# Kernel optimization log

Hardware: AMD Instinct MI355X
Metric: run time of the kernel (lower is better)

## Reference

```python
import jax, jax.numpy as jnp
import numpy as np
from jax import lax

EPS = 1e-6
NUM_BANDS = 128


def setup_inputs() -> dict:
    key = jax.random.key(0)
    kx, = jax.random.split(key, 1)
    B, C, F, T = 32, 1, NUM_BANDS, 6000
    x = jax.random.uniform(kx, (B, C, F, T), dtype=jnp.float32)  # nonneg spectrogram energies
    # parameters per band, initialized as in PCEN.__init__ (s=0.025, alpha=delta=r=1.0)
    log_s = jnp.full((F,), np.log(0.025), dtype=jnp.float32)
    log_alpha = jnp.zeros((F,), dtype=jnp.float32)
    log_delta = jnp.zeros((F,), dtype=jnp.float32)
    log_r = jnp.zeros((F,), dtype=jnp.float32)
    return {"x": x, "log_s": log_s, "log_alpha": log_alpha,
            "log_delta": log_delta, "log_r": log_r}


def _pcen(x, log_s, log_alpha, log_delta, log_r):
    # x: (B, C, bands, T)
    s = jnp.exp(log_s)  # (bands,)
    xt = jnp.moveaxis(x, -1, 0)  # (T, B, C, bands) time-major for the scan
    init = xt[0]  # init_smoother_from_data=True -> M_0 = X_0

    def step(m, xf):
        m_new = (1.0 - s) * m + s * xf
        return m_new, m_new

    _, ms = lax.scan(step, init, xt[1:])  # (T-1, B, C, bands)
    smoother = jnp.concatenate([init[None], ms], axis=0)  # (T, B, C, bands)
    smoother = jnp.moveaxis(smoother, 0, -1)  # (B, C, bands, T)

    alpha = jnp.exp(log_alpha)[:, None]  # (bands, 1)
    delta = jnp.exp(log_delta)[:, None]
    r = jnp.exp(log_r)[:, None]
    # (eps + M)^(-alpha) computed stably: exp(-alpha * (log eps + log1p(M/eps)))
    gain = jnp.exp(-alpha * (jnp.log(EPS) + jnp.log1p(smoother / EPS)))
    return (x * gain + delta) ** r - delta ** r


def reference(x, log_s, log_alpha, log_delta, log_r):
    return _pcen(x, log_s, log_alpha, log_delta, log_r)
```

## Files before the change

kernel.cpp:

```cpp
#include <hip/hip_runtime.h>

#define TLEN     6000
#define NV4      1500
#define CHUNK_V4 256
#define NCHUNK   6
#define V4PL     4
#define EPT      16
#define EPS      1e-6f
#define LN_EPS   (-13.815511f)
#define INV_EPS  1e6f

__device__ __forceinline__ float pcen_full(float xv, float M, float alpha,
                                           float delta, float r, float deltar) {
    float gain = __expf(-alpha * (LN_EPS + __logf(fmaf(M, INV_EPS, 1.0f))));
    return __powf(fmaf(xv, gain, delta), r) - deltar;
}

__device__ __forceinline__ float ipow6(float b, int e) {
    float r = 1.0f;
    #pragma unroll
    for (int i = 0; i < 6; ++i) {
        if (e & 1) r *= b;
        b *= b;
        e >>= 1;
    }
    return r;
}

__global__ __launch_bounds__(256, 4) void pcen_kernel(
    const float* __restrict__ x,
    const float* __restrict__ log_s,
    const float* __restrict__ log_alpha,
    const float* __restrict__ log_delta,
    const float* __restrict__ log_r,
    float* __restrict__ out,
    int num_series, int F)
{
    const int g    = (int)((blockIdx.x * blockDim.x + threadIdx.x) >> 6);
    const int lane = (int)(threadIdx.x & 63);
    if (g >= num_series * NCHUNK) return;
    const int series = g / NCHUNK;
    const int c      = g - series * NCHUNK;
    const int f      = series % F;

    const float la = log_alpha[f], ld = log_delta[f], lr = log_r[f];
    const bool  triv = (la == 0.0f) && (ld == 0.0f) && (lr == 0.0f);

    const float s    = __expf(log_s[f]);
    const float oms  = 1.0f - s;

    float pw[EPT + 1];
    pw[0] = 1.0f;
    #pragma unroll
    for (int k = 1; k <= EPT; ++k) pw[k] = pw[k - 1] * oms;
    const float oms4  = pw[4];
    const float omsP  = pw[16];

    float A_chunk = omsP;
    #pragma unroll
    for (int i = 0; i < 6; ++i) A_chunk *= A_chunk;
    const bool decay_ok = fabsf(A_chunk) < 1e-7f;

    const float wl = ipow6(omsP, 63 - lane);

    const float alpha  = __expf(la);
    const float delta  = __expf(ld);
    const float r      = __expf(lr);
    const float deltar = __powf(delta, lr == 0.0f ? 1.0f : r);

    const float4* __restrict__ xb = (const float4*)(x + (size_t)series * TLEN);
    float4* __restrict__ ob       = (float4*)(out + (size_t)series * TLEN);

    const int tb = c * CHUNK_V4 + 4 * lane;
    const int wb = (c - 1) * CHUNK_V4 + 4 * lane;
    float4 wq[V4PL], q[V4PL];
    if (c > 0) {
        #pragma unroll
        for (int j = 0; j < V4PL; ++j) wq[j] = xb[wb + j];
    }
    #pragma unroll
    for (int j = 0; j < V4PL; ++j)
        q[j] = (tb + j < NV4) ? xb[tb + j] : make_float4(0.f, 0.f, 0.f, 0.f);

    float Mc = 0.0f;

    if (!decay_ok) {
        for (int wc = 0; wc + 1 < c; ++wc) {
            const int b0 = wc * CHUNK_V4 + 4 * lane;
            float B = 0.0f;
            #pragma unroll
            for (int j = 0; j < V4PL; ++j) {
                const float4 xq = xb[b0 + j];
                const float c0 = (wc == 0 && lane == 0 && j == 0) ? 1.0f : s;
                B = fmaf(oms, B, c0 * xq.x);
                B = fmaf(oms, B, s  * xq.y);
                B = fmaf(oms, B, s  * xq.z);
                B = fmaf(oms, B, s  * xq.w);
            }
            float v = wl * B;
            #pragma unroll
            for (int off = 1; off < 64; off <<= 1)
                v += __shfl_xor(v, off, 64);
            Mc = fmaf(A_chunk, Mc, v);
        }
    }

    if (c > 0) {
        float B = 0.0f;
        #pragma unroll
        for (int j = 0; j < V4PL; ++j) {
            const float4 xq = wq[j];
            const float c0 = (c == 1 && lane == 0 && j == 0) ? 1.0f : s;
            B = fmaf(oms, B, c0 * xq.x);
            B = fmaf(oms, B, s  * xq.y);
            B = fmaf(oms, B, s  * xq.z);
            B = fmaf(oms, B, s  * xq.w);
        }
        float v = wl * B;
        #pragma unroll
        for (int off = 1; off < 64; off <<= 1)
            v += __shfl_xor(v, off, 64);
        Mc = fmaf(A_chunk, Mc, v);
    }

    float Bv[EPT];
    float B = 0.0f, A = 1.0f;
    #pragma unroll
    for (int j = 0; j < V4PL; ++j) {
        if (tb + j < NV4) {
            const float4 xq = q[j];
            const float c0 = (c == 0 && lane == 0 && j == 0) ? 1.0f : s;
            B = fmaf(oms, B, c0 * xq.x); Bv[4 * j + 0] = B;
            B = fmaf(oms, B, s  * xq.y); Bv[4 * j + 1] = B;
            B = fmaf(oms, B, s  * xq.z); Bv[4 * j + 2] = B;
            B = fmaf(oms, B, s  * xq.w); Bv[4 * j + 3] = B;
            A *= oms4;
        }
    }

    #pragma unroll
    for (int off = 1; off < 64; off <<= 1) {
        const float Ap = __shfl_up(A, off, 64);
        const float Bp = __shfl_up(B, off, 64);
        if (lane >= off) { B = fmaf(A, Bp, B); A = A * Ap; }
    }
    float Ae = __shfl_up(A, 1, 64);
    float Be = __shfl_up(B, 1, 64);
    if (lane == 0) { Ae = 1.0f; Be = 0.0f; }

    const float Min = fmaf(Ae, Mc, Be);

    if (triv) {
        #pragma unroll
        for (int j = 0; j < V4PL; ++j) {
            if (tb + j < NV4) {
                const float4 xq = q[j];
                float4 o; float m;
                m = fmaf(pw[4 * j + 1], Min, Bv[4 * j + 0]);
                o.x = xq.x * __builtin_amdgcn_rcpf(m + EPS);
                m = fmaf(pw[4 * j + 2], Min, Bv[4 * j + 1]);
                o.y = xq.y * __builtin_amdgcn_rcpf(m + EPS);
                m = fmaf(pw[4 * j + 3], Min, Bv[4 * j + 2]);
                o.z = xq.z * __builtin_amdgcn_rcpf(m + EPS);
                m = fmaf(pw[4 * j + 4], Min, Bv[4 * j + 3]);
                o.w = xq.w * __builtin_amdgcn_rcpf(m + EPS);
                ob[tb + j] = o;
            }
        }
    } else {
        #pragma unroll
        for (int j = 0; j < V4PL; ++j) {
            if (tb + j < NV4) {
                const float4 xq = q[j];
                float4 o; float m;
                m = fmaf(pw[4 * j + 1], Min, Bv[4 * j + 0]);
                o.x = pcen_full(xq.x, m, alpha, delta, r, deltar);
                m = fmaf(pw[4 * j + 2], Min, Bv[4 * j + 1]);
                o.y = pcen_full(xq.y, m, alpha, delta, r, deltar);
                m = fmaf(pw[4 * j + 3], Min, Bv[4 * j + 2]);
                o.z = pcen_full(xq.z, m, alpha, delta, r, deltar);
                m = fmaf(pw[4 * j + 4], Min, Bv[4 * j + 3]);
                o.w = pcen_full(xq.w, m, alpha, delta, r, deltar);
                ob[tb + j] = o;
            }
        }
    }
}

extern "C" void kernel_launch(void* const* d_in, const int* in_sizes, int n_in,
                              void* d_out, int out_size, void* d_ws, size_t ws_size,
                              hipStream_t stream) {
    const float* x         = (const float*)d_in[0];
    const float* log_s     = (const float*)d_in[1];
    const float* log_alpha = (const float*)d_in[2];
    const float* log_delta = (const float*)d_in[3];
    const float* log_r     = (const float*)d_in[4];
    float* out             = (float*)d_out;

    const int F = in_sizes[1];
    const int num_series = in_sizes[0] / TLEN;
    const int num_waves  = num_series * NCHUNK;
    const int num_threads = num_waves * 64;
    const int grid = (num_threads + 255) / 256;

    pcen_kernel<<<grid, 256, 0, stream>>>(x, log_s, log_alpha, log_delta, log_r,
                                          out, num_series, F);
}
```

Before: 187.5 us.

## Process each series in two halves with sequential chunk carry and prefetch

Each wave now handles three consecutive 256-float4 chunks of one half-series instead of one chunk, passing the chunk-end smoother value forward so no warm-up reads are needed except a single lookback chunk for the second half. The per-chunk scan drops the A-coefficient shuffle by using geometric weights, and outputs are recomputed by a serial recurrence from the chunk-entry value rather than by storing per-element prefix values. The next chunk's loads are issued before the current chunk is computed, and launch bounds ask for higher occupancy. This cuts redundant global reads and shuffle work but leaves far fewer waves (8192) and more serial work per wave.

Result: slower. 247.1 us (+31.8%).

```diff
diff --git a/kernel.cpp b/kernel.cpp
--- a/kernel.cpp
+++ b/kernel.cpp
@@ -3,9 +3,7 @@
 #define TLEN     6000
 #define NV4      1500
 #define CHUNK_V4 256
-#define NCHUNK   6
-#define V4PL     4
-#define EPT      16
+#define HALF_V4  768
 #define EPS      1e-6f
 #define LN_EPS   (-13.815511f)
 #define INV_EPS  1e6f
@@ -27,7 +25,77 @@
     return r;
 }
 
-__global__ __launch_bounds__(256, 4) void pcen_kernel(
+template<bool PARTIAL>
+__device__ __forceinline__ float chunk_compute(
+    const float4 (&q)[4], const int fb, const int lane, const bool finit,
+    const float s, const float oms, const float omsP, const float Apow,
+    const float A64, const bool triv,
+    const float la, const float ld, const float lr,
+    const float Mc, float4* __restrict__ ob)
+{
+    float B = 0.0f;
+    #pragma unroll
+    for (int j = 0; j < 4; ++j) {
+        if (!PARTIAL || (fb + j < NV4)) {
+            const float c0 = (finit && lane == 0 && j == 0) ? 1.0f : s;
+            B = fmaf(oms, B, c0 * q[j].x);
+            B = fmaf(oms, B, s  * q[j].y);
+            B = fmaf(oms, B, s  * q[j].z);
+            B = fmaf(oms, B, s  * q[j].w);
+        }
+    }
+
+    float S = B;
+    float w = omsP;
+    #pragma unroll
+    for (int off = 1; off < 64; off <<= 1) {
+        const float Sp = __shfl_up(S, off, 64);
+        if (lane >= off) S = fmaf(w, Sp, S);
+        w *= w;
+    }
+    const float Se  = __shfl_up(S, 1, 64);
+    const float Be  = (lane == 0) ? 0.0f : Se;
+    const float Min = fmaf(Apow, Mc, Be);
+
+    float McNext = 0.0f;
+    if (!PARTIAL) McNext = fmaf(A64, Mc, __shfl(S, 63, 64));
+
+    float m = Min;
+    if (triv) {
+        #pragma unroll
+        for (int j = 0; j < 4; ++j) {
+            if (!PARTIAL || (fb + j < NV4)) {
+                const float c0 = (finit && lane == 0 && j == 0) ? 1.0f : s;
+                float4 o;
+                m = fmaf(oms, m, c0 * q[j].x); o.x = q[j].x * __builtin_amdgcn_rcpf(m + EPS);
+                m = fmaf(oms, m, s  * q[j].y); o.y = q[j].y * __builtin_amdgcn_rcpf(m + EPS);
+                m = fmaf(oms, m, s  * q[j].z); o.z = q[j].z * __builtin_amdgcn_rcpf(m + EPS);
+                m = fmaf(oms, m, s  * q[j].w); o.w = q[j].w * __builtin_amdgcn_rcpf(m + EPS);
+                ob[fb + j] = o;
+            }
+        }
+    } else {
+        const float alpha  = __expf(la);
+        const float delta  = __expf(ld);
+        const float r      = __expf(lr);
+        const float deltar = __powf(delta, lr == 0.0f ? 1.0f : r);
+        #pragma unroll
+        for (int j = 0; j < 4; ++j) {
+            if (!PARTIAL || (fb + j < NV4)) {
+                const float c0 = (finit && lane == 0 && j == 0) ? 1.0f : s;
+                float4 o;
+                m = fmaf(oms, m, c0 * q[j].x); o.x = pcen_full(q[j].x, m, alpha, delta, r, deltar);
+                m = fmaf(oms, m, s  * q[j].y); o.y = pcen_full(q[j].y, m, alpha, delta, r, deltar);
+                m = fmaf(oms, m, s  * q[j].z); o.z = pcen_full(q[j].z, m, alpha, delta, r, deltar);
+                m = fmaf(oms, m, s  * q[j].w); o.w = pcen_full(q[j].w, m, alpha, delta, r, deltar);
+                ob[fb + j] = o;
+            }
+        }
+    }
+    return McNext;
+}
+
+__global__ __launch_bounds__(256, 8) void pcen_kernel(
     const float* __restrict__ x,
     const float* __restrict__ log_s,
     const float* __restrict__ log_alpha,
@@ -38,9 +106,9 @@
 {
     const int g    = (int)((blockIdx.x * blockDim.x + threadIdx.x) >> 6);
     const int lane = (int)(threadIdx.x & 63);
-    if (g >= num_series * NCHUNK) return;
-    const int series = g / NCHUNK;
-    const int c      = g - series * NCHUNK;
+    if (g >= num_series * 2) return;
+    const int series = g >> 1;
+    const int h      = g & 1;
     const int f      = series % F;
 
     const float la = log_alpha[f], ld = log_delta[f], lr = log_r[f];
@@ -48,143 +116,86 @@
 
     const float s    = __expf(log_s[f]);
     const float oms  = 1.0f - s;
-
-    float pw[EPT + 1];
-    pw[0] = 1.0f;
-    #pragma unroll
-    for (int k = 1; k <= EPT; ++k) pw[k] = pw[k - 1] * oms;
-    const float oms4  = pw[4];
-    const float omsP  = pw[16];
-
-    float A_chunk = omsP;
-    #pragma unroll
-    for (int i = 0; i < 6; ++i) A_chunk *= A_chunk;
-    const bool decay_ok = fabsf(A_chunk) < 1e-7f;
-
-    const float wl = ipow6(omsP, 63 - lane);
-
-    const float alpha  = __expf(la);
-    const float delta  = __expf(ld);
-    const float r      = __expf(lr);
-    const float deltar = __powf(delta, lr == 0.0f ? 1.0f : r);
+    const float oms2 = oms * oms;
+    const float oms4 = oms2 * oms2;
+    const float oms8 = oms4 * oms4;
+    const float omsP = oms8 * oms8;
+
+    float A64 = omsP;
+    #pragma unroll
+    for (int i = 0; i < 6; ++i) A64 *= A64;
+    const bool decay_ok = fabsf(A64) < 1e-7f;
+
+    const float Apow = ipow6(omsP, lane);
 
     const float4* __restrict__ xb = (const float4*)(x + (size_t)series * TLEN);
     float4* __restrict__ ob       = (float4*)(out + (size_t)series * TLEN);
 
-    const int tb = c * CHUNK_V4 + 4 * lane;
-    const int wb = (c - 1) * CHUNK_V4 + 4 * lane;
-    float4 wq[V4PL], q[V4PL];
-    if (c > 0) {
+    const int hb = h * HALF_V4;
+    const int l4 = 4 * lane;
+
+    float4 bufA[4], bufB[4];
+
+    #pragma unroll
+    for (int j = 0; j < 4; ++j) bufA[j] = xb[hb + l4 + j];
+
+    float Mc = 0.0f;
+    if (h == 1) {
+        const float wl = ipow6(omsP, 63 - lane);
+        if (decay_ok) {
+            #pragma unroll
+            for (int j = 0; j < 4; ++j) bufB[j] = xb[(HALF_V4 - CHUNK_V4) + l4 + j];
+            float Bw = 0.0f;
+            #pragma unroll
+            for (int j = 0; j < 4; ++j) {
+                const float4 qw = bufB[j];
+                Bw = fmaf(oms, Bw, s * qw.x);
+                Bw = fmaf(oms, Bw, s * qw.y);
+                Bw = fmaf(oms, Bw, s * qw.z);
+                Bw = fmaf(oms, Bw, s * qw.w);
+            }
+            float v = wl * Bw;
+            #pragma unroll
+            for (int off = 1; off < 64; off <<= 1) v += __shfl_xor(v, off, 64);
+            Mc = v;
+        } else {
+            for (int wc = 0; wc < 3; ++wc) {
+                float Bw = 0.0f;
+                #pragma unroll
+                for (int j = 0; j < 4; ++j) {
+                    const float4 qw = xb[wc * CHUNK_V4 + l4 + j];
+                    const float c0 = (wc == 0 && lane == 0 && j == 0) ? 1.0f : s;
+                    Bw = fmaf(oms, Bw, c0 * qw.x);
+                    Bw = fmaf(oms, Bw, s  * qw.y);
+                    Bw = fmaf(oms, Bw, s  * qw.z);
+                    Bw = fmaf(oms, Bw, s  * qw.w);
+                }
+                float v = wl * Bw;
+                #pragma unroll
+                for (int off = 1; off < 64; off <<= 1) v += __shfl_xor(v, off, 64);
+                Mc = fmaf(A64, Mc, v);
+            }
+        }
+    }
+
+    #pragma unroll
+    for (int j = 0; j < 4; ++j) bufB[j] = xb[hb + CHUNK_V4 + l4 + j];
+
+    Mc = chunk_compute<false>(bufA, hb + l4, lane, (h == 0),
+                              s, oms, omsP, Apow, A64, triv, la, ld, lr, Mc, ob);
+
+    {
+        const int fb2 = hb + 2 * CHUNK_V4 + l4;
         #pragma unroll
-        for (int j = 0; j < V4PL; ++j) wq[j] = xb[wb + j];
-    }
-    #pragma unroll
-    for (int j = 0; j < V4PL; ++j)
-        q[j] = (tb + j < NV4) ? xb[tb + j] : make_float4(0.f, 0.f, 0.f, 0.f);
-
-    float Mc = 0.0f;
-
-    if (!decay_ok) {
-        for (int wc = 0; wc + 1 < c; ++wc) {
-            const int b0 = wc * CHUNK_V4 + 4 * lane;
-            float B = 0.0f;
-            #pragma unroll
-            for (int j = 0; j < V4PL; ++j) {
-                const float4 xq = xb[b0 + j];
-                const float c0 = (wc == 0 && lane == 0 && j == 0) ? 1.0f : s;
-                B = fmaf(oms, B, c0 * xq.x);
-                B = fmaf(oms, B, s  * xq.y);
-                B = fmaf(oms, B, s  * xq.z);
-                B = fmaf(oms, B, s  * xq.w);
-            }
-            float v = wl * B;
-            #pragma unroll
-            for (int off = 1; off < 64; off <<= 1)
-                v += __shfl_xor(v, off, 64);
-            Mc = fmaf(A_chunk, Mc, v);
-        }
-    }
-
-    if (c > 0) {
-        float B = 0.0f;
-        #pragma unroll
-        for (int j = 0; j < V4PL; ++j) {
-            const float4 xq = wq[j];
-            const float c0 = (c == 1 && lane == 0 && j == 0) ? 1.0f : s;
-            B = fmaf(oms, B, c0 * xq.x);
-            B = fmaf(oms, B, s  * xq.y);
-            B = fmaf(oms, B, s  * xq.z);
-            B = fmaf(oms, B, s  * xq.w);
-        }
-        float v = wl * B;
-        #pragma unroll
-        for (int off = 1; off < 64; off <<= 1)
-            v += __shfl_xor(v, off, 64);
-        Mc = fmaf(A_chunk, Mc, v);
-    }
-
-    float Bv[EPT];
-    float B = 0.0f, A = 1.0f;
-    #pragma unroll
-    for (int j = 0; j < V4PL; ++j) {
-        if (tb + j < NV4) {
-            const float4 xq = q[j];
-            const float c0 = (c == 0 && lane == 0 && j == 0) ? 1.0f : s;
-            B = fmaf(oms, B, c0 * xq.x); Bv[4 * j + 0] = B;
-            B = fmaf(oms, B, s  * xq.y); Bv[4 * j + 1] = B;
-            B = fmaf(oms, B, s  * xq.z); Bv[4 * j + 2] = B;
-            B = fmaf(oms, B, s  * xq.w); Bv[4 * j + 3] = B;
-            A *= oms4;
-        }
-    }
-
-    #pragma unroll
-    for (int off = 1; off < 64; off <<= 1) {
-        const float Ap = __shfl_up(A, off, 64);
-        const float Bp = __shfl_up(B, off, 64);
-        if (lane >= off) { B = fmaf(A, Bp, B); A = A * Ap; }
-    }
-    float Ae = __shfl_up(A, 1, 64);
-    float Be = __shfl_up(B, 1, 64);
-    if (lane == 0) { Ae = 1.0f; Be = 0.0f; }
-
-    const float Min = fmaf(Ae, Mc, Be);
-
-    if (triv) {
-        #pragma unroll
-        for (int j = 0; j < V4PL; ++j) {
-            if (tb + j < NV4) {
-                const float4 xq = q[j];
-                float4 o; float m;
-                m = fmaf(pw[4 * j + 1], Min, Bv[4 * j + 0]);
-                o.x = xq.x * __builtin_amdgcn_rcpf(m + EPS);
-                m = fmaf(pw[4 * j + 2], Min, Bv[4 * j + 1]);
-                o.y = xq.y * __builtin_amdgcn_rcpf(m + EPS);
-                m = fmaf(pw[4 * j + 3], Min, Bv[4 * j + 2]);
-                o.z = xq.z * __builtin_amdgcn_rcpf(m + EPS);
-                m = fmaf(pw[4 * j + 4], Min, Bv[4 * j + 3]);
-                o.w = xq.w * __builtin_amdgcn_rcpf(m + EPS);
-                ob[tb + j] = o;
-            }
-        }
-    } else {
-        #pragma unroll
-        for (int j = 0; j < V4PL; ++j) {
-            if (tb + j < NV4) {
-                const float4 xq = q[j];
-                float4 o; float m;
-                m = fmaf(pw[4 * j + 1], Min, Bv[4 * j + 0]);
-                o.x = pcen_full(xq.x, m, alpha, delta, r, deltar);
-                m = fmaf(pw[4 * j + 2], Min, Bv[4 * j + 1]);
-                o.y = pcen_full(xq.y, m, alpha, delta, r, deltar);
-                m = fmaf(pw[4 * j + 3], Min, Bv[4 * j + 2]);
-                o.z = pcen_full(xq.z, m, alpha, delta, r, deltar);
-                m = fmaf(pw[4 * j + 4], Min, Bv[4 * j + 3]);
-                o.w = pcen_full(xq.w, m, alpha, delta, r, deltar);
-                ob[tb + j] = o;
-            }
-        }
-    }
+        for (int j = 0; j < 4; ++j)
+            bufA[j] = (fb2 + j < NV4) ? xb[fb2 + j] : make_float4(0.f, 0.f, 0.f, 0.f);
+    }
+
+    Mc = chunk_compute<false>(bufB, hb + CHUNK_V4 + l4, lane, false,
+                              s, oms, omsP, Apow, A64, triv, la, ld, lr, Mc, ob);
+
+    chunk_compute<true>(bufA, hb + 2 * CHUNK_V4 + l4, lane, false,
+                        s, oms, omsP, Apow, A64, triv, la, ld, lr, Mc, ob);
 }
 
 extern "C" void kernel_launch(void* const* d_in, const int* in_sizes, int n_in,
@@ -199,7 +210,7 @@
 
     const int F = in_sizes[1];
     const int num_series = in_sizes[0] / TLEN;
-    const int num_waves  = num_series * NCHUNK;
+    const int num_waves  = num_series * 2;
     const int num_threads = num_waves * 64;
     const int grid = (num_threads + 255) / 256;
 
```
